# Kernel tuning notes

Hardware: AMD Instinct MI355X
Metric: run time of the kernel (lower is better)

## Reference

```python
import jax, jax.numpy as jnp
import numpy as np

N, E = 50000, 800000
NODE_DIM, EDGE_DIM, HIDDEN = 128, 32, 128


def setup_inputs() -> dict:
    key = jax.random.key(0)
    ks = jax.random.split(key, 12)
    def lin(k, fan_in, shape):
        bound = 1.0 / np.sqrt(fan_in)
        return jax.random.uniform(k, shape, jnp.float32, -bound, bound)
    return {
        "x": jax.random.normal(ks[0], (N, NODE_DIM), jnp.float32),
        "edge_index": jax.random.randint(ks[1], (2, E), 0, N),
        "edge_attr": jax.random.normal(ks[2], (E, EDGE_DIM), jnp.float32),
        # msg MLP: Linear(node+edge -> hidden), Linear(hidden -> hidden)
        "W1": lin(ks[3], NODE_DIM + EDGE_DIM, (HIDDEN, NODE_DIM + EDGE_DIM)),
        "b1": lin(ks[4], NODE_DIM + EDGE_DIM, (HIDDEN,)),
        "W2": lin(ks[5], HIDDEN, (HIDDEN, HIDDEN)),
        "b2": lin(ks[6], HIDDEN, (HIDDEN,)),
        # GRUCell(input=HIDDEN, hidden=NODE_DIM); gate order r,z,n (torch)
        "W_ih": lin(ks[7], NODE_DIM, (3 * NODE_DIM, HIDDEN)),
        "b_ih": lin(ks[8], NODE_DIM, (3 * NODE_DIM,)),
        "W_hh": lin(ks[9], NODE_DIM, (3 * NODE_DIM, NODE_DIM)),
        "b_hh": lin(ks[10], NODE_DIM, (3 * NODE_DIM,)),
    }


def reference(x, edge_index, edge_attr, W1, b1, W2, b2, W_ih, b_ih, W_hh, b_hh):
    src, dst = edge_index[0], edge_index[1]
    # gather + edge MLP: [E, node+edge] -> [E, hidden]
    m_in = jnp.concatenate([x[src], edge_attr], axis=-1)
    h1 = jax.nn.silu(m_in @ W1.T + b1)
    m = jax.nn.silu(h1 @ W2.T + b2)
    # scatter-add messages per destination node
    agg = jax.ops.segment_sum(m, dst, num_segments=x.shape[0])  # [N, hidden]
    # GRUCell: gates in torch order (r, z, n)
    gi = agg @ W_ih.T + b_ih  # [N, 3*node_dim]
    gh = x @ W_hh.T + b_hh
    i_r, i_z, i_n = jnp.split(gi, 3, axis=-1)
    h_r, h_z, h_n = jnp.split(gh, 3, axis=-1)
    r = jax.nn.sigmoid(i_r + h_r)
    z = jax.nn.sigmoid(i_z + h_z)
    n = jnp.tanh(i_n + r * h_n)
    return (1.0 - z) * n + z * x
```

## Files before the change

kernel.cpp:

```cpp
#include <hip/hip_runtime.h>
#include <hip/hip_bf16.h>
#include <cstdint>

typedef __bf16 bf16x8 __attribute__((ext_vector_type(8)));
typedef __bf16 bf16x4 __attribute__((ext_vector_type(4)));
typedef float  f32x4  __attribute__((ext_vector_type(4)));

#define ND 128
#define HID 128

__device__ __forceinline__ f32x4 mfma_bf16(bf16x8 a, bf16x8 b, f32x4 c) {
  return __builtin_amdgcn_mfma_f32_16x16x32_bf16(a, b, c, 0, 0, 0);
}
__device__ __forceinline__ float fast_sigmoid(float x) {
  return __fdividef(1.f, 1.f + __expf(-x));
}
__device__ __forceinline__ float fast_silu(float x) {
  return __fdividef(x, 1.f + __expf(-x));
}
__device__ __forceinline__ float fast_tanh(float x) {
  float cx = fminf(fmaxf(x, -15.f), 15.f);
  float e = __expf(2.f * cx);
  return __fdividef(e - 1.f, e + 1.f);
}

__global__ void cvt_all(const float* __restrict__ s0, __bf16* __restrict__ d0, int c1,
                        const float* __restrict__ s1, __bf16* __restrict__ d1, int c2,
                        const float* __restrict__ s2, __bf16* __restrict__ d2, int c3,
                        const float* __restrict__ s3, __bf16* __restrict__ d3, int c4,
                        const float* __restrict__ s4, __bf16* __restrict__ d4, int c5) {
  int i = blockIdx.x * blockDim.x + threadIdx.x;
  const float* s; __bf16* d; int j;
  if (i < c1)      { s = s0; d = d0; j = i; }
  else if (i < c2) { s = s1; d = d1; j = i - c1; }
  else if (i < c3) { s = s2; d = d2; j = i - c2; }
  else if (i < c4) { s = s3; d = d3; j = i - c3; }
  else if (i < c5) { s = s4; d = d4; j = i - c4; }
  else return;
  const float4* sp = reinterpret_cast<const float4*>(s) + (size_t)j * 2;
  float4 a = sp[0], b = sp[1];
  bf16x8 v;
  v[0] = (__bf16)a.x; v[1] = (__bf16)a.y; v[2] = (__bf16)a.z; v[3] = (__bf16)a.w;
  v[4] = (__bf16)b.x; v[5] = (__bf16)b.y; v[6] = (__bf16)b.z; v[7] = (__bf16)b.w;
  reinterpret_cast<bf16x8*>(d)[j] = v;
}

__global__ void k_hist(const int* __restrict__ dst, int* __restrict__ counts, int E) {
  int e = blockIdx.x * 256 + threadIdx.x;
  if (e < E) atomicAdd(&counts[dst[e]], 1);
}

__global__ void k_blocksum(const int* __restrict__ counts, int* __restrict__ bsum) {
  __shared__ int sd[256];
  int t = threadIdx.x;
  sd[t] = counts[blockIdx.x * 256 + t];
  __syncthreads();
  for (int d = 128; d > 0; d >>= 1) { if (t < d) sd[t] += sd[t + d]; __syncthreads(); }
  if (!t) bsum[blockIdx.x] = sd[0];
}

__global__ void k_scan_bsum(int* __restrict__ bsum, int nb) {
  __shared__ int sd[256];
  int t = threadIdx.x;
  int v = (t < nb) ? bsum[t] : 0;
  sd[t] = v;
  __syncthreads();
  for (int d = 1; d < 256; d <<= 1) {
    int u = (t >= d) ? sd[t - d] : 0;
    __syncthreads();
    sd[t] += u;
    __syncthreads();
  }
  if (t < nb) bsum[t] = sd[t] - v;
}

__global__ void k_scan_write(const int* __restrict__ counts, const int* __restrict__ bsum,
                             int* __restrict__ cursor) {
  __shared__ int sd[256];
  int t = threadIdx.x, b = blockIdx.x;
  int i = b * 256 + t;
  int c = counts[i];
  sd[t] = c;
  __syncthreads();
  for (int d = 1; d < 256; d <<= 1) {
    int u = (t >= d) ? sd[t - d] : 0;
    __syncthreads();
    sd[t] += u;
    __syncthreads();
  }
  cursor[i] = bsum[b] + sd[t] - c;
}

__global__ void k_perm(const int* __restrict__ dst, int* __restrict__ cursor,
                       int* __restrict__ eperm, int* __restrict__ dsorted, int E) {
  int e = blockIdx.x * 256 + threadIdx.x;
  if (e < E) {
    int d = dst[e];
    int p = atomicAdd(&cursor[d], 1);
    eperm[p] = e;
    dsorted[p] = d;
  }
}

#define TILE_E 64

__global__ __launch_bounds__(512, 4) void edge_mlp7(
    const __bf16* __restrict__ xb,
    const int*    __restrict__ srcp,
    const float*  __restrict__ ea,
    const __bf16* __restrict__ W1b,
    const float*  __restrict__ b1,
    const __bf16* __restrict__ W2b,
    const float*  __restrict__ b2,
    const int*    __restrict__ eperm,
    const int*    __restrict__ dsorted,
    float* __restrict__ agg,
    int ntiles)
{
  __shared__ __bf16 Als[TILE_E * 160];
  __shared__ __bf16 H1[TILE_E * 128];
  __shared__ int dstls[TILE_E];
  char* AB = (char*)Als;
  char* HB = (char*)H1;

  const int tid = threadIdx.x;
  const int w  = tid >> 6;
  const int l  = tid & 63;
  const int l4 = l >> 4;
  const int lm = l & 15;
  const int jb = w * 16;

  bf16x8 bw1[5], bw2[4];
  {
    const int jr = jb + lm;
#pragma unroll
    for (int kt = 0; kt < 5; ++kt)
      bw1[kt] = *reinterpret_cast<const bf16x8*>(W1b + (size_t)jr * 160 + kt * 32 + l4 * 8);
#pragma unroll
    for (int kt = 0; kt < 4; ++kt)
      bw2[kt] = *reinterpret_cast<const bf16x8*>(W2b + (size_t)jr * 128 + kt * 32 + l4 * 8);
  }
  const float4 b1v = *reinterpret_cast<const float4*>(b1 + jb + l4 * 4);
  const float4 b2v = *reinterpret_cast<const float4*>(b2 + jb + l4 * 4);

  const int xslot = tid >> 4, xq = tid & 15;
  const int aslot = tid >> 3, aq = tid & 7;

  bf16x8 pxv0 = {}, pxv1 = {};
  float4 pea_ = {};
  int pdst_ = 0;

  auto PREFETCH = [&](int t) {
    int p0 = t * TILE_E;
    int e0i = eperm[p0 + xslot];
    int e1i = eperm[p0 + xslot + 32];
    int s0 = srcp[e0i];
    int s1 = srcp[e1i];
    pxv0 = *reinterpret_cast<const bf16x8*>(xb + (size_t)s0 * ND + xq * 8);
    pxv1 = *reinterpret_cast<const bf16x8*>(xb + (size_t)s1 * ND + xq * 8);
    int e2i = eperm[p0 + aslot];
    pea_ = reinterpret_cast<const float4*>(ea)[(size_t)e2i * 8 + aq];
    if (tid < TILE_E) pdst_ = dsorted[p0 + tid];
  };

  int tile = blockIdx.x;
  if (tile < ntiles) PREFETCH(tile);

  for (; tile < ntiles; tile += gridDim.x) {
    __syncthreads();

    {
      int s_ = xslot;
      *reinterpret_cast<bf16x8*>(AB + s_ * 320 + ((xq ^ (s_ & 7)) << 4)) = pxv0;
      int s2 = xslot + 32;
      *reinterpret_cast<bf16x8*>(AB + s2 * 320 + ((xq ^ (s2 & 7)) << 4)) = pxv1;
    }
    {
      bf16x4 h;
      h[0] = (__bf16)pea_.x; h[1] = (__bf16)pea_.y;
      h[2] = (__bf16)pea_.z; h[3] = (__bf16)pea_.w;
      int pc = 16 + ((aq >> 1) ^ (aslot & 3));
      *reinterpret_cast<bf16x4*>(AB + aslot * 320 + (pc << 4) + ((aq & 1) << 3)) = h;
    }
    if (tid < TILE_E) dstls[tid] = pdst_;
    __syncthreads();

    int nt = tile + gridDim.x;
    if (nt < ntiles) PREFETCH(nt);

#pragma unroll
    for (int et = 0; et < 4; ++et) {
      const int s_ = et * 16 + lm;
      const int sw = s_ & 7;
      f32x4 acc = {0.f, 0.f, 0.f, 0.f};
#pragma unroll
      for (int kt = 0; kt < 4; ++kt) {
        bf16x8 bfrag = *reinterpret_cast<const bf16x8*>(AB + s_ * 320 + (((kt * 4 + l4) ^ sw) << 4));
        acc = mfma_bf16(bw1[kt], bfrag, acc);
      }
      {
        bf16x8 bfrag = *reinterpret_cast<const bf16x8*>(AB + s_ * 320 + ((16 + (l4 ^ (s_ & 3))) << 4));
        acc = mfma_bf16(bw1[4], bfrag, acc);
      }
      bf16x4 h0;
#pragma unroll
      for (int rr = 0; rr < 4; ++rr)
        h0[rr] = (__bf16)fast_silu(acc[rr] + (&b1v.x)[rr]);
      int c0 = w * 2 + (l4 >> 1);
      int inner = (l4 & 1) << 3;
      *reinterpret_cast<bf16x4*>(HB + s_ * 256 + ((c0 ^ sw) << 4) + inner) = h0;
    }
    __syncthreads();

#pragma unroll
    for (int et = 0; et < 4; ++et) {
      const int s_ = et * 16 + lm;
      const int sw = s_ & 7;
      f32x4 acc = {0.f, 0.f, 0.f, 0.f};
#pragma unroll
      for (int kt = 0; kt < 4; ++kt) {
        bf16x8 bfrag = *reinterpret_cast<const bf16x8*>(HB + s_ * 256 + (((kt * 4 + l4) ^ sw) << 4));
        acc = mfma_bf16(bw2[kt], bfrag, acc);
      }
      bf16x4 m0;
#pragma unroll
      for (int rr = 0; rr < 4; ++rr)
        m0[rr] = (__bf16)fast_silu(acc[rr] + (&b2v.x)[rr]);
      int c0 = w * 2 + (l4 >> 1);
      int inner = (l4 & 1) << 3;
      *reinterpret_cast<bf16x4*>(AB + s_ * 256 + ((c0 ^ sw) << 4) + inner) = m0;
    }
    __syncthreads();

    if (w < 4) {
      const int base = w * 16;
      int myd = dstls[base + (l & 15)];
      float a0 = 0.f, a1 = 0.f;
      int cur = __builtin_amdgcn_readlane(myd, 0);
#pragma unroll
      for (int i = 0; i < 16; ++i) {
        int nd = __builtin_amdgcn_readlane(myd, i);
        if (nd != cur) {
          atomicAdd(agg + (size_t)cur * HID + l * 2, a0);
          atomicAdd(agg + (size_t)cur * HID + l * 2 + 1, a1);
          a0 = 0.f; a1 = 0.f; cur = nd;
        }
        int ss = base + i;
        uint32_t u = *reinterpret_cast<const uint32_t*>(
            AB + ss * 256 + (((l >> 2) ^ (ss & 7)) << 4) + ((l & 3) << 2));
        a0 += __uint_as_float(u << 16);
        a1 += __uint_as_float(u & 0xffff0000u);
      }
      atomicAdd(agg + (size_t)cur * HID + l * 2, a0);
      atomicAdd(agg + (size_t)cur * HID + l * 2 + 1, a1);
    }
  }
}

__global__ __launch_bounds__(512) void gru3(
    const float*  __restrict__ agg,
    const __bf16* __restrict__ xb,
    const float*  __restrict__ x,
    const __bf16* __restrict__ Wih, const float* __restrict__ bih,
    const __bf16* __restrict__ Whh, const float* __restrict__ bhh,
    float* __restrict__ out, int N, int ntilesN)
{
  const int tid = threadIdx.x;
  const int w = tid >> 6, l = tid & 63;
  const int l4 = l >> 4, lm = l & 15;
  const int jb = w * 16;
  const int jr = jb + lm, jz = jr + 128, jn = jr + 256;

  bf16x8 WiR[4], WhR[4], WiZ[4], WhZ[4], WiN[4], WhN[4];
#pragma unroll
  for (int kt = 0; kt < 4; ++kt) {
    int ko = kt * 32 + l4 * 8;
    WiR[kt] = *reinterpret_cast<const bf16x8*>(Wih + (size_t)jr * ND + ko);
    WhR[kt] = *reinterpret_cast<const bf16x8*>(Whh + (size_t)jr * ND + ko);
    WiZ[kt] = *reinterpret_cast<const bf16x8*>(Wih + (size_t)jz * ND + ko);
    WhZ[kt] = *reinterpret_cast<const bf16x8*>(Whh + (size_t)jz * ND + ko);
    WiN[kt] = *reinterpret_cast<const bf16x8*>(Wih + (size_t)jn * ND + ko);
    WhN[kt] = *reinterpret_cast<const bf16x8*>(Whh + (size_t)jn * ND + ko);
  }
  float4 birv, bizv, binv, bhnv;
  {
    int j0 = jb + l4 * 4;
    float4 a = *reinterpret_cast<const float4*>(bih + j0);
    float4 b = *reinterpret_cast<const float4*>(bhh + j0);
    birv = make_float4(a.x + b.x, a.y + b.y, a.z + b.z, a.w + b.w);
    a = *reinterpret_cast<const float4*>(bih + 128 + j0);
    b = *reinterpret_cast<const float4*>(bhh + 128 + j0);
    bizv = make_float4(a.x + b.x, a.y + b.y, a.z + b.z, a.w + b.w);
    binv = *reinterpret_cast<const float4*>(bih + 256 + j0);
    bhnv = *reinterpret_cast<const float4*>(bhh + 256 + j0);
  }

  for (int bt = blockIdx.x; bt < ntilesN; bt += gridDim.x) {
    const int n0 = bt * 64;
#pragma unroll
    for (int rt = 0; rt < 4; ++rt) {
      const int node = n0 + rt * 16 + lm;
      const bool ok = node < N;
      bf16x8 aA[4], aX[4];
#pragma unroll
      for (int kt = 0; kt < 4; ++kt) {
        int ko = kt * 32 + l4 * 8;
        bf16x8 z8 = {};
        if (ok) {
          float4 a0 = *reinterpret_cast<const float4*>(agg + (size_t)node * ND + ko);
          float4 a1 = *reinterpret_cast<const float4*>(agg + (size_t)node * ND + ko + 4);
          bf16x8 v;
          v[0] = (__bf16)a0.x; v[1] = (__bf16)a0.y; v[2] = (__bf16)a0.z; v[3] = (__bf16)a0.w;
          v[4] = (__bf16)a1.x; v[5] = (__bf16)a1.y; v[6] = (__bf16)a1.z; v[7] = (__bf16)a1.w;
          aA[kt] = v;
          aX[kt] = *reinterpret_cast<const bf16x8*>(xb + (size_t)node * ND + ko);
        } else {
          aA[kt] = z8;
          aX[kt] = z8;
        }
      }
      f32x4 aR = {0.f,0.f,0.f,0.f}, aZ = {0.f,0.f,0.f,0.f};
      f32x4 ai = {0.f,0.f,0.f,0.f}, ah = {0.f,0.f,0.f,0.f};
#pragma unroll
      for (int kt = 0; kt < 4; ++kt) {
        aR = mfma_bf16(WiR[kt], aA[kt], aR);
        aR = mfma_bf16(WhR[kt], aX[kt], aR);
        aZ = mfma_bf16(WiZ[kt], aA[kt], aZ);
        aZ = mfma_bf16(WhZ[kt], aX[kt], aZ);
        ai = mfma_bf16(WiN[kt], aA[kt], ai);
        ah = mfma_bf16(WhN[kt], aX[kt], ah);
      }
      if (ok) {
        float4 xv = *reinterpret_cast<const float4*>(x + (size_t)node * ND + jb + l4 * 4);
        float4 ov;
#pragma unroll
        for (int rr = 0; rr < 4; ++rr) {
          float r = fast_sigmoid(aR[rr] + (&birv.x)[rr]);
          float z = fast_sigmoid(aZ[rr] + (&bizv.x)[rr]);
          float n = fast_tanh(ai[rr] + (&binv.x)[rr] + r * (ah[rr] + (&bhnv.x)[rr]));
          (&ov.x)[rr] = (1.f - z) * n + z * (&xv.x)[rr];
        }
        *reinterpret_cast<float4*>(out + (size_t)node * ND + jb + l4 * 4) = ov;
      }
    }
  }
}

extern "C" void kernel_launch(void* const* d_in, const int* in_sizes, int n_in,
                              void* d_out, int out_size, void* d_ws, size_t ws_size,
                              hipStream_t stream) {
  const float* x   = (const float*)d_in[0];
  const int*   ei  = (const int*)d_in[1];
  const float* ea  = (const float*)d_in[2];
  const float* W1  = (const float*)d_in[3];
  const float* b1  = (const float*)d_in[4];
  const float* W2  = (const float*)d_in[5];
  const float* b2  = (const float*)d_in[6];
  const float* Wih = (const float*)d_in[7];
  const float* bih = (const float*)d_in[8];
  const float* Whh = (const float*)d_in[9];
  const float* bhh = (const float*)d_in[10];
  float* out = (float*)d_out;
  const int N = in_sizes[0] / ND;
  const int E = in_sizes[1] / 2;

  const int nb = (N + 255) / 256;
  const int nC = nb * 256;

  char* ws = (char*)d_ws;
  size_t off = 0;
  auto alloc = [&](size_t bytes) -> void* {
    void* p = ws + off;
    off += (bytes + 255) & ~(size_t)255;
    return p;
  };
  __bf16* xb      = (__bf16*)alloc((size_t)N * ND * 2);
  __bf16* W1b     = (__bf16*)alloc(128 * 160 * 2);
  __bf16* W2b     = (__bf16*)alloc(128 * 128 * 2);
  __bf16* Wihb    = (__bf16*)alloc(384 * 128 * 2);
  __bf16* Whhb    = (__bf16*)alloc(384 * 128 * 2);
  int*    counts  = (int*)alloc((size_t)nC * 4);
  int*    cursor  = (int*)alloc((size_t)nC * 4);
  int*    bsum    = (int*)alloc(256 * 4);
  int*    eperm   = (int*)alloc((size_t)E * 4);
  int*    dsorted = (int*)alloc((size_t)E * 4);
  float*  agg     = (float*)alloc((size_t)N * ND * 4);
  (void)ws_size;

  const int* srcp = ei;
  const int* dstp = ei + E;

  hipMemsetAsync(agg, 0, (size_t)N * ND * 4, stream);
  hipMemsetAsync(counts, 0, (size_t)nC * 4, stream);

  const int n8_x = N * ND / 8, n8_1 = 128 * 160 / 8, n8_2 = 128 * 128 / 8, n8_g = 384 * 128 / 8;
  int c1 = n8_x, c2 = c1 + n8_1, c3 = c2 + n8_2, c4 = c3 + n8_g, c5 = c4 + n8_g;
  cvt_all<<<(c5 + 255) / 256, 256, 0, stream>>>(x, xb, c1, W1, W1b, c2, W2, W2b, c3,
                                                Wih, Wihb, c4, Whh, Whhb, c5);

  k_hist<<<(E + 255) / 256, 256, 0, stream>>>(dstp, counts, E);
  k_blocksum<<<nb, 256, 0, stream>>>(counts, bsum);
  k_scan_bsum<<<1, 256, 0, stream>>>(bsum, nb);
  k_scan_write<<<nb, 256, 0, stream>>>(counts, bsum, cursor);
  k_perm<<<(E + 255) / 256, 256, 0, stream>>>(dstp, cursor, eperm, dsorted, E);

  const int ntiles = E / TILE_E;
  edge_mlp7<<<2500, 512, 0, stream>>>(xb, srcp, ea, W1b, b1, W2b, b2,
                                      eperm, dsorted, agg, ntiles);

  const int ntilesN = (N + 63) / 64;
  gru3<<<256, 512, 0, stream>>>(agg, xb, x, Wihb, bih, Whhb, bhh, out, N, ntilesN);
}
```

Baseline: 350.7 us.

## Fuse memsets into prep kernel, pack edge info, swizzle tiles by XCD

The two memsets are folded into the bf16 conversion kernel to save launches. k_perm now writes a packed int4 (src, dst, edge id) per sorted edge, which removes the dependent eperm→src indirection in the edge kernel's prefetch. Tile assignment is remapped so that consecutive tiles land on the same XCD, which improves L2 locality for agg atomics on the sorted destinations. The MFMA section also raises wave priority with s_setprio. The packed int4 costs more bytes written per edge than the two int arrays it replaces.

```diff
diff --git a/kernel.cpp b/kernel.cpp
--- a/kernel.cpp
+++ b/kernel.cpp
@@ -24,25 +24,42 @@
   return __fdividef(e - 1.f, e + 1.f);
 }
 
-__global__ void cvt_all(const float* __restrict__ s0, __bf16* __restrict__ d0, int c1,
-                        const float* __restrict__ s1, __bf16* __restrict__ d1, int c2,
-                        const float* __restrict__ s2, __bf16* __restrict__ d2, int c3,
-                        const float* __restrict__ s3, __bf16* __restrict__ d3, int c4,
-                        const float* __restrict__ s4, __bf16* __restrict__ d4, int c5) {
+__global__ void k_prep(const float* __restrict__ s0, __bf16* __restrict__ d0, int c1,
+                       const float* __restrict__ s1, __bf16* __restrict__ d1, int c2,
+                       const float* __restrict__ s2, __bf16* __restrict__ d2, int c3,
+                       const float* __restrict__ s3, __bf16* __restrict__ d3, int c4,
+                       const float* __restrict__ s4, __bf16* __restrict__ d4, int c5,
+                       float* __restrict__ agg, int aggz,
+                       int* __restrict__ counts, int cntz) {
   int i = blockIdx.x * blockDim.x + threadIdx.x;
-  const float* s; __bf16* d; int j;
-  if (i < c1)      { s = s0; d = d0; j = i; }
-  else if (i < c2) { s = s1; d = d1; j = i - c1; }
-  else if (i < c3) { s = s2; d = d2; j = i - c2; }
-  else if (i < c4) { s = s3; d = d3; j = i - c3; }
-  else if (i < c5) { s = s4; d = d4; j = i - c4; }
-  else return;
-  const float4* sp = reinterpret_cast<const float4*>(s) + (size_t)j * 2;
-  float4 a = sp[0], b = sp[1];
-  bf16x8 v;
-  v[0] = (__bf16)a.x; v[1] = (__bf16)a.y; v[2] = (__bf16)a.z; v[3] = (__bf16)a.w;
-  v[4] = (__bf16)b.x; v[5] = (__bf16)b.y; v[6] = (__bf16)b.z; v[7] = (__bf16)b.w;
-  reinterpret_cast<bf16x8*>(d)[j] = v;
+  if (i < c5) {
+    const float* s; __bf16* d; int j;
+    if (i < c1)      { s = s0; d = d0; j = i; }
+    else if (i < c2) { s = s1; d = d1; j = i - c1; }
+    else if (i < c3) { s = s2; d = d2; j = i - c2; }
+    else if (i < c4) { s = s3; d = d3; j = i - c3; }
+    else             { s = s4; d = d4; j = i - c4; }
+    const float4* sp = reinterpret_cast<const float4*>(s) + (size_t)j * 2;
+    float4 a = sp[0], b = sp[1];
+    bf16x8 v;
+    v[0] = (__bf16)a.x; v[1] = (__bf16)a.y; v[2] = (__bf16)a.z; v[3] = (__bf16)a.w;
+    v[4] = (__bf16)b.x; v[5] = (__bf16)b.y; v[6] = (__bf16)b.z; v[7] = (__bf16)b.w;
+    reinterpret_cast<bf16x8*>(d)[j] = v;
+    return;
+  }
+  int k = i - c5;
+  if (k < aggz) {
+    float4 z = make_float4(0.f, 0.f, 0.f, 0.f);
+    float4* p = reinterpret_cast<float4*>(agg) + (size_t)k * 2;
+    p[0] = z; p[1] = z;
+    return;
+  }
+  k -= aggz;
+  if (k < cntz) {
+    int4 z = make_int4(0, 0, 0, 0);
+    int4* p = reinterpret_cast<int4*>(counts) + (size_t)k * 2;
+    p[0] = z; p[1] = z;
+  }
 }
 
 __global__ void k_hist(const int* __restrict__ dst, int* __restrict__ counts, int E) {
@@ -91,29 +108,26 @@
   cursor[i] = bsum[b] + sd[t] - c;
 }
 
-__global__ void k_perm(const int* __restrict__ dst, int* __restrict__ cursor,
-                       int* __restrict__ eperm, int* __restrict__ dsorted, int E) {
+__global__ void k_perm(const int* __restrict__ src, const int* __restrict__ dst,
+                       int* __restrict__ cursor, int4* __restrict__ einfo, int E) {
   int e = blockIdx.x * 256 + threadIdx.x;
   if (e < E) {
     int d = dst[e];
     int p = atomicAdd(&cursor[d], 1);
-    eperm[p] = e;
-    dsorted[p] = d;
+    einfo[p] = make_int4(src[e], d, e, 0);
   }
 }
 
 #define TILE_E 64
 
-__global__ __launch_bounds__(512, 4) void edge_mlp7(
+__global__ __launch_bounds__(512, 4) void edge_mlp8(
     const __bf16* __restrict__ xb,
-    const int*    __restrict__ srcp,
     const float*  __restrict__ ea,
     const __bf16* __restrict__ W1b,
     const float*  __restrict__ b1,
     const __bf16* __restrict__ W2b,
     const float*  __restrict__ b2,
-    const int*    __restrict__ eperm,
-    const int*    __restrict__ dsorted,
+    const int4*   __restrict__ einfo,
     float* __restrict__ agg,
     int ntiles)
 {
@@ -152,18 +166,21 @@
 
   auto PREFETCH = [&](int t) {
     int p0 = t * TILE_E;
-    int e0i = eperm[p0 + xslot];
-    int e1i = eperm[p0 + xslot + 32];
-    int s0 = srcp[e0i];
-    int s1 = srcp[e1i];
+    int s0 = einfo[p0 + xslot].x;
+    int s1 = einfo[p0 + xslot + 32].x;
     pxv0 = *reinterpret_cast<const bf16x8*>(xb + (size_t)s0 * ND + xq * 8);
     pxv1 = *reinterpret_cast<const bf16x8*>(xb + (size_t)s1 * ND + xq * 8);
-    int e2i = eperm[p0 + aslot];
-    pea_ = reinterpret_cast<const float4*>(ea)[(size_t)e2i * 8 + aq];
-    if (tid < TILE_E) pdst_ = dsorted[p0 + tid];
+    int e2 = einfo[p0 + aslot].z;
+    pea_ = reinterpret_cast<const float4*>(ea)[(size_t)e2 * 8 + aq];
+    if (tid < TILE_E) pdst_ = einfo[p0 + tid].y;
   };
 
-  int tile = blockIdx.x;
+  int nwg = gridDim.x;
+  int q = nwg >> 3, r = nwg & 7;
+  int xcd = blockIdx.x & 7, pos = blockIdx.x >> 3;
+  int swz = (xcd < r ? xcd * (q + 1) : r * (q + 1) + (xcd - r) * q) + pos;
+
+  int tile = swz;
   if (tile < ntiles) PREFETCH(tile);
 
   for (; tile < ntiles; tile += gridDim.x) {
@@ -188,6 +205,7 @@
     int nt = tile + gridDim.x;
     if (nt < ntiles) PREFETCH(nt);
 
+    __builtin_amdgcn_s_setprio(1);
 #pragma unroll
     for (int et = 0; et < 4; ++et) {
       const int s_ = et * 16 + lm;
@@ -230,6 +248,7 @@
       int inner = (l4 & 1) << 3;
       *reinterpret_cast<bf16x4*>(AB + s_ * 256 + ((c0 ^ sw) << 4) + inner) = m0;
     }
+    __builtin_amdgcn_s_setprio(0);
     __syncthreads();
 
     if (w < 4) {
@@ -382,31 +401,31 @@
   int*    counts  = (int*)alloc((size_t)nC * 4);
   int*    cursor  = (int*)alloc((size_t)nC * 4);
   int*    bsum    = (int*)alloc(256 * 4);
-  int*    eperm   = (int*)alloc((size_t)E * 4);
-  int*    dsorted = (int*)alloc((size_t)E * 4);
+  int4*   einfo   = (int4*)alloc((size_t)E * 16);
   float*  agg     = (float*)alloc((size_t)N * ND * 4);
   (void)ws_size;
 
   const int* srcp = ei;
   const int* dstp = ei + E;
 
-  hipMemsetAsync(agg, 0, (size_t)N * ND * 4, stream);
-  hipMemsetAsync(counts, 0, (size_t)nC * 4, stream);
-
   const int n8_x = N * ND / 8, n8_1 = 128 * 160 / 8, n8_2 = 128 * 128 / 8, n8_g = 384 * 128 / 8;
   int c1 = n8_x, c2 = c1 + n8_1, c3 = c2 + n8_2, c4 = c3 + n8_g, c5 = c4 + n8_g;
-  cvt_all<<<(c5 + 255) / 256, 256, 0, stream>>>(x, xb, c1, W1, W1b, c2, W2, W2b, c3,
-                                                Wih, Wihb, c4, Whh, Whhb, c5);
+  int aggz = N * ND / 8;
+  int cntz = nC / 8;
+  int prep_total = c5 + aggz + cntz;
+  k_prep<<<(prep_total + 255) / 256, 256, 0, stream>>>(
+      x, xb, c1, W1, W1b, c2, W2, W2b, c3, Wih, Wihb, c4, Whh, Whhb, c5,
+      agg, aggz, counts, cntz);
 
   k_hist<<<(E + 255) / 256, 256, 0, stream>>>(dstp, counts, E);
   k_blocksum<<<nb, 256, 0, stream>>>(counts, bsum);
   k_scan_bsum<<<1, 256, 0, stream>>>(bsum, nb);
   k_scan_write<<<nb, 256, 0, stream>>>(counts, bsum, cursor);
-  k_perm<<<(E + 255) / 256, 256, 0, stream>>>(dstp, cursor, eperm, dsorted, E);
+  k_perm<<<(E + 255) / 256, 256, 0, stream>>>(srcp, dstp, cursor, einfo, E);
 
   const int ntiles = E / TILE_E;
-  edge_mlp7<<<2500, 512, 0, stream>>>(xb, srcp, ea, W1b, b1, W2b, b2,
-                                      eperm, dsorted, agg, ntiles);
+  edge_mlp8<<<2500, 512, 0, stream>>>(xb, ea, W1b, b1, W2b, b2,
+                                      einfo, agg, ntiles);
 
   const int ntilesN = (N + 63) / 64;
   gru3<<<256, 512, 0, stream>>>(agg, xb, x, Wihb, bih, Whhb, bhh, out, N, ntilesN);
```

After: 339.5 us. 1.03x faster.
